# Kernel tuning notes

Hardware: AMD Instinct MI355X
Metric: run time of the kernel (lower is better)

## Reference

```python
import jax, jax.numpy as jnp
import numpy as np

N_NODES = 100000
N_EDGES = 800000
HIDDEN = 256
BOTTLENECK = 32


def setup_inputs() -> dict:
    key = jax.random.key(0)
    k1, k2, k3, k4 = jax.random.split(key, 4)
    x = jax.random.normal(k1, (N_NODES, HIDDEN), dtype=jnp.float32)
    edge_index = jax.random.randint(k2, (2, N_EDGES), 0, N_NODES, dtype=jnp.int64)
    # PyG GCNConv linear weights, init per module: normal(std=1e-5), zero bias
    W_down = jax.random.normal(k3, (BOTTLENECK, HIDDEN), dtype=jnp.float32) * 1e-5
    b_down = jnp.zeros((BOTTLENECK,), dtype=jnp.float32)
    W_up = jax.random.normal(k4, (HIDDEN, BOTTLENECK), dtype=jnp.float32) * 1e-5
    b_up = jnp.zeros((HIDDEN,), dtype=jnp.float32)
    return {"x": x, "edge_index": edge_index, "W_down": W_down, "b_down": b_down,
            "W_up": W_up, "b_up": b_up}


def reference(x, edge_index, W_down, b_down, W_up, b_up):
    N = x.shape[0]
    loops = jnp.arange(N, dtype=edge_index.dtype)
    # gcn_norm with self-loops (edge weight = 1), symmetric normalization
    row = jnp.concatenate([edge_index[0], loops])  # source nodes
    col = jnp.concatenate([edge_index[1], loops])  # target nodes
    deg = jax.ops.segment_sum(jnp.ones(row.shape[0], dtype=x.dtype), col, num_segments=N)
    dinv = jnp.where(deg > 0, jax.lax.rsqrt(deg), 0.0)
    norm = dinv[row] * dinv[col]  # [E+N]

    def gcn_conv(h, W, b):
        h = h @ W.T                                   # [N, out]
        msgs = h[row] * norm[:, None]                 # gather + weight
        return jax.ops.segment_sum(msgs, col, num_segments=N) + b

    h = jax.nn.relu(gcn_conv(x, W_down, b_down))      # down-proj conv + act
    out = gcn_conv(h, W_up, b_up) + x                 # up-proj conv + skip
    return out
```

## Files before the change

kernel.cpp:

```cpp
#include <hip/hip_runtime.h>
#include <hip/hip_bf16.h>
#include <stdint.h>

#define HID 256
#define BOT 32

typedef short short8 __attribute__((ext_vector_type(8)));
typedef unsigned short ushort8 __attribute__((ext_vector_type(8)));
typedef float floatx4 __attribute__((ext_vector_type(4)));

__device__ __forceinline__ unsigned short f2bu(float f) {
    return (unsigned short)(__float_as_uint(f) >> 16);
}
__device__ __forceinline__ float bu2f(unsigned short u) {
    return __uint_as_float((unsigned int)u << 16);
}
__device__ __forceinline__ short8 pack8(float4 a, float4 b) {
    short8 r;
    r[0] = (short)f2bu(a.x); r[1] = (short)f2bu(a.y);
    r[2] = (short)f2bu(a.z); r[3] = (short)f2bu(a.w);
    r[4] = (short)f2bu(b.x); r[5] = (short)f2bu(b.y);
    r[6] = (short)f2bu(b.z); r[7] = (short)f2bu(b.w);
    return r;
}

__device__ __forceinline__ int detect_mode(const int* __restrict__ ei, int* smode) {
    if (threadIdx.x < 64) {
        int found = 0;
        #pragma unroll
        for (int i = 0; i < 8; ++i) {
            int slot = 2 * (threadIdx.x * 8 + i) + 1;
            if (ei[slot] != 0) found = 1;
        }
        unsigned long long b = __ballot(found);
        if (threadIdx.x == 0) *smode = (b == 0ULL) ? 1 : 0;
    }
    __syncthreads();
    return *smode;
}


__global__ __launch_bounds__(256) void k_deg(const int* __restrict__ ei, int E,
                                             int* __restrict__ deg) {
    __shared__ int smode;
    int mode = detect_mode(ei, &smode);
    int e = blockIdx.x * 256 + threadIdx.x;
    if (e >= E) return;
    int d = mode ? ei[2 * (size_t)E + 2 * e] : ei[(size_t)E + e];
    atomicAdd(deg + d, 1);
}

__global__ __launch_bounds__(256) void k_alloc(const int* __restrict__ deg,
                                               float* __restrict__ dinv,
                                               int* __restrict__ start,
                                               int* __restrict__ cur,
                                               int* __restrict__ cursor, int N) {
    __shared__ int sdata[256];
    __shared__ int sbase;
    int tid = threadIdx.x;
    int i = blockIdx.x * 256 + tid;
    int d = (i < N) ? deg[i] : 0;
    if (i < N) dinv[i] = rsqrtf((float)(d + 1));
    sdata[tid] = d;
    __syncthreads();
    for (int off = 1; off < 256; off <<= 1) {
        int t = (tid >= off) ? sdata[tid - off] : 0;
        __syncthreads();
        sdata[tid] += t;
        __syncthreads();
    }
    if (tid == 0) sbase = atomicAdd(cursor, sdata[255]);
    __syncthreads();
    if (i < N) {
        int st = sbase + sdata[tid] - d;
        start[i] = st;
        cur[i] = st;
    }
}

__global__ __launch_bounds__(256) void k_fill_gemm(
    const int* __restrict__ ei, int E,
    const float* __restrict__ dinv, int* __restrict__ cur,
    int2* __restrict__ srcw,
    const float* __restrict__ x, const float* __restrict__ Wd,
    unsigned short* __restrict__ P, int N, int gemmBlocks, int gemmWaves)
{
    if (blockIdx.x >= gemmBlocks) {
        __shared__ int smode;
        int mode = detect_mode(ei, &smode);
        int e = (blockIdx.x - gemmBlocks) * 256 + threadIdx.x;
        if (e >= E) return;
        int s, d;
        if (mode) { s = ei[2 * (size_t)e]; d = ei[2 * (size_t)E + 2 * e]; }
        else      { s = ei[(size_t)e];     d = ei[(size_t)E + e]; }
        float w = dinv[s] * dinv[d];
        int slot = atomicAdd(cur + d, 1);
        srcw[slot] = make_int2(s, __float_as_int(w));
        return;
    }

    int wid  = (blockIdx.x * 256 + threadIdx.x) >> 6;
    int lane = threadIdx.x & 63;
    int m = lane & 15, q = lane >> 4;

    short8 bfr[2][8];
    #pragma unroll
    for (int jt = 0; jt < 2; ++jt) {
        const float4* wr = (const float4*)(Wd + (size_t)(jt * 16 + m) * HID);
        #pragma unroll
        for (int ks = 0; ks < 8; ++ks) {
            int c = (ks * 32 + q * 8) >> 2;
            bfr[jt][ks] = pack8(wr[c], wr[c + 1]);
        }
    }

    int tiles = (N + 15) >> 4;
    for (int t = wid; t < tiles; t += gemmWaves) {
        int n0 = t << 4;
        int row = n0 + m; if (row >= N) row = N - 1;
        const float4* xr = (const float4*)(x + (size_t)row * HID);
        floatx4 acc0 = {0.f, 0.f, 0.f, 0.f};
        floatx4 acc1 = {0.f, 0.f, 0.f, 0.f};
        #pragma unroll
        for (int ks = 0; ks < 8; ++ks) {
            int c = (ks * 32 + q * 8) >> 2;
            short8 af = pack8(xr[c], xr[c + 1]);
            acc0 = __builtin_amdgcn_mfma_f32_16x16x32_bf16(bfr[0][ks], af, acc0, 0, 0, 0);
            acc1 = __builtin_amdgcn_mfma_f32_16x16x32_bf16(bfr[1][ks], af, acc1, 0, 0, 0);
        }
        if (n0 + m < N) {
            unsigned int* pr = (unsigned int*)(P + (size_t)(n0 + m) * BOT);
            uint2 v0, v1;
            v0.x = (unsigned int)f2bu(acc0[0]) | ((unsigned int)f2bu(acc0[1]) << 16);
            v0.y = (unsigned int)f2bu(acc0[2]) | ((unsigned int)f2bu(acc0[3]) << 16);
            v1.x = (unsigned int)f2bu(acc1[0]) | ((unsigned int)f2bu(acc1[1]) << 16);
            v1.y = (unsigned int)f2bu(acc1[2]) | ((unsigned int)f2bu(acc1[3]) << 16);
            *(uint2*)(pr + q * 2)     = v0;
            *(uint2*)(pr + 8 + q * 2) = v1;
        }
    }
}

__global__ __launch_bounds__(256) void k_gather(
    const unsigned short* __restrict__ feat, const float* __restrict__ dinv,
    const int* __restrict__ start, const int* __restrict__ endp,
    const int2* __restrict__ srcw, const float* __restrict__ bias,
    unsigned short* __restrict__ dst, int N, int relu_bias)
{
    int t = blockIdx.x * 256 + threadIdx.x;
    int n = t >> 2, jq = (t & 3) * 8;
    if (n >= N) return;
    float di = dinv[n];
    float w0 = di * di;
    float acc[8];
    ushort8 sv = *(const ushort8*)(feat + (size_t)n * BOT + jq);
    #pragma unroll
    for (int i = 0; i < 8; ++i) acc[i] = w0 * bu2f(sv[i]);
    int k = start[n], en = endp[n];
    while (k < en) {
        int2 p[4];
        #pragma unroll
        for (int u = 0; u < 4; ++u) {
            int kk = k + u;
            int safe = kk < en ? kk : en - 1;
            p[u] = srcw[safe];
            if (kk >= en) p[u].y = 0;
        }
        ushort8 f[4];
        #pragma unroll
        for (int u = 0; u < 4; ++u)
            f[u] = *(const ushort8*)(feat + (size_t)p[u].x * BOT + jq);
        #pragma unroll
        for (int u = 0; u < 4; ++u) {
            float w = __int_as_float(p[u].y);
            #pragma unroll
            for (int i = 0; i < 8; ++i) acc[i] += w * bu2f(f[u][i]);
        }
        k += 4;
    }
    if (relu_bias) {
        #pragma unroll
        for (int i = 0; i < 8; ++i) {
            float a = acc[i] + bias[jq + i];
            acc[i] = a > 0.f ? a : 0.f;
        }
    }
    ushort8 o;
    #pragma unroll
    for (int i = 0; i < 8; ++i) o[i] = f2bu(acc[i]);
    *(ushort8*)(dst + (size_t)n * BOT + jq) = o;
}

__global__ __launch_bounds__(256) void k_gather_out(
    const unsigned short* __restrict__ A1, const float* __restrict__ dinv,
    const int* __restrict__ start, const int* __restrict__ endp,
    const int2* __restrict__ srcw,
    const float* __restrict__ x, const float* __restrict__ Wup,
    const float* __restrict__ bup, float* __restrict__ out, int N)
{
    int gw   = (blockIdx.x * 256 + threadIdx.x) >> 6;
    int lane = threadIdx.x & 63;
    int m = lane & 15, q = lane >> 4, jq = q * 8;
    int tiles = (N + 15) >> 4;
    if (gw >= tiles) return;
    int n0 = gw << 4;
    int n = n0 + m;
    bool ok = n < N;
    int nc = ok ? n : N - 1;

    float di = dinv[nc];
    float w0 = di * di;
    float acc[8];
    ushort8 sv = *(const ushort8*)(A1 + (size_t)nc * BOT + jq);
    #pragma unroll
    for (int i = 0; i < 8; ++i) acc[i] = w0 * bu2f(sv[i]);
    int k = start[nc], en = endp[nc];
    while (k < en) {
        int2 p[4];
        #pragma unroll
        for (int u = 0; u < 4; ++u) {
            int kk = k + u;
            int safe = kk < en ? kk : en - 1;
            p[u] = srcw[safe];
            if (kk >= en) p[u].y = 0;
        }
        ushort8 f[4];
        #pragma unroll
        for (int u = 0; u < 4; ++u)
            f[u] = *(const ushort8*)(A1 + (size_t)p[u].x * BOT + jq);
        #pragma unroll
        for (int u = 0; u < 4; ++u) {
            float w = __int_as_float(p[u].y);
            #pragma unroll
            for (int i = 0; i < 8; ++i) acc[i] += w * bu2f(f[u][i]);
        }
        k += 4;
    }

    short8 af;
    #pragma unroll
    for (int i = 0; i < 8; ++i) af[i] = (short)f2bu(acc[i]);

    const float4* xrow = (const float4*)(x + (size_t)nc * HID);
    floatx4* orow = (floatx4*)(out + (size_t)nc * HID);
    #pragma unroll
    for (int ft = 0; ft < 16; ++ft) {
        const float4* wr = (const float4*)(Wup + (size_t)(ft * 16 + m) * BOT);
        short8 bfr = pack8(wr[q * 2], wr[q * 2 + 1]);
        floatx4 a = {0.f, 0.f, 0.f, 0.f};
        a = __builtin_amdgcn_mfma_f32_16x16x32_bf16(bfr, af, a, 0, 0, 0);
        if (ok) {
            int c = ft * 4 + q;
            float4 xv = xrow[c];
            float4 bb = *(const float4*)(bup + ft * 16 + q * 4);
            floatx4 res;
            res[0] = a[0] + bb.x + xv.x;
            res[1] = a[1] + bb.y + xv.y;
            res[2] = a[2] + bb.z + xv.z;
            res[3] = a[3] + bb.w + xv.w;
            __builtin_nontemporal_store(res, &orow[c]);
        }
    }
}

extern "C" void kernel_launch(void* const* d_in, const int* in_sizes, int n_in,
                              void* d_out, int out_size, void* d_ws, size_t ws_size,
                              hipStream_t stream) {
    const float* x  = (const float*)d_in[0];
    const int*   ei = (const int*)d_in[1];
    const float* Wd = (const float*)d_in[2];
    const float* bd = (const float*)d_in[3];
    const float* Wu = (const float*)d_in[4];
    const float* bu = (const float*)d_in[5];
    float* out = (float*)d_out;

    int N = in_sizes[0] / HID;
    int E = in_sizes[1] / 2;

    char* ws = (char*)d_ws;
    int*   flags = (int*)ws;
    int*   deg   = (int*)(ws + 16);
    float* dinv  = (float*)(ws + 16 + (size_t)N * 4);
    int*   startp= (int*)(ws + 16 + (size_t)N * 8);
    int*   curp  = (int*)(ws + 16 + (size_t)N * 12);
    int2*  srcw  = (int2*)(ws + 16 + (size_t)N * 16);
    unsigned short* P  = (unsigned short*)(ws + 16 + (size_t)N * 16 + (size_t)E * 8);
    unsigned short* A1 = (unsigned short*)(ws + 16 + (size_t)N * 16 + (size_t)E * 8 + (size_t)N * 64);

    (void)hipMemsetAsync(ws, 0, 16 + (size_t)N * 4, stream);

    int eblocks = (E + 255) / 256;
    k_deg<<<eblocks, 256, 0, stream>>>(ei, E, deg);

    k_alloc<<<(N + 255) / 256, 256, 0, stream>>>(deg, dinv, startp, curp, flags + 1, N);

    int tiles = (N + 15) / 16;
    int gemmBlocks = (tiles + 3) / 4;
    k_fill_gemm<<<gemmBlocks + eblocks, 256, 0, stream>>>(
        ei, E, dinv, curp, srcw, x, Wd, P, N, gemmBlocks, gemmBlocks * 4);

    int gthreads = N * 4;
    k_gather<<<(gthreads + 255) / 256, 256, 0, stream>>>(P, dinv, startp, curp, srcw, bd, A1, N, 1);

    int oblocks = (tiles + 3) / 4;
    k_gather_out<<<oblocks, 256, 0, stream>>>(A1, dinv, startp, curp, srcw, x, Wu, bu, out, N);
}
```

Measured before the change: 353.5 us.

## Record per-edge slot during degree count to drop fill-phase atomics; split GEMM kernel

The degree-counting kernel now stores the return value of its atomicAdd as a per-edge slot. The CSR fill kernel computes each edge's position as start[dst] + slot instead of doing a second atomic on a cursor array. The cursor array is dropped, and the gather kernels take the end offset from start plus degree. The fused fill+GEMM launch is split into a separate fill kernel and a down-projection GEMM kernel with a fixed grid of 782 blocks. This adds an extra per-edge int array to write and read, and one more kernel launch.

New measurement: 349.2 us. Within noise of the previous version (-1.2%).

```diff
diff --git a/kernel.cpp b/kernel.cpp
--- a/kernel.cpp
+++ b/kernel.cpp
@@ -41,19 +41,19 @@
 
 
 __global__ __launch_bounds__(256) void k_deg(const int* __restrict__ ei, int E,
-                                             int* __restrict__ deg) {
+                                             int* __restrict__ deg,
+                                             int* __restrict__ eslot) {
     __shared__ int smode;
     int mode = detect_mode(ei, &smode);
     int e = blockIdx.x * 256 + threadIdx.x;
     if (e >= E) return;
     int d = mode ? ei[2 * (size_t)E + 2 * e] : ei[(size_t)E + e];
-    atomicAdd(deg + d, 1);
+    eslot[e] = atomicAdd(deg + d, 1);
 }
 
 __global__ __launch_bounds__(256) void k_alloc(const int* __restrict__ deg,
                                                float* __restrict__ dinv,
                                                int* __restrict__ start,
-                                               int* __restrict__ cur,
                                                int* __restrict__ cursor, int N) {
     __shared__ int sdata[256];
     __shared__ int sbase;
@@ -71,34 +71,30 @@
     }
     if (tid == 0) sbase = atomicAdd(cursor, sdata[255]);
     __syncthreads();
-    if (i < N) {
-        int st = sbase + sdata[tid] - d;
-        start[i] = st;
-        cur[i] = st;
-    }
-}
-
-__global__ __launch_bounds__(256) void k_fill_gemm(
-    const int* __restrict__ ei, int E,
-    const float* __restrict__ dinv, int* __restrict__ cur,
-    int2* __restrict__ srcw,
+    if (i < N) start[i] = sbase + sdata[tid] - d;
+}
+
+__global__ __launch_bounds__(256) void k_fill(const int* __restrict__ ei, int E,
+                                              const float* __restrict__ dinv,
+                                              const int* __restrict__ start,
+                                              const int* __restrict__ eslot,
+                                              int2* __restrict__ srcw) {
+    __shared__ int smode;
+    int mode = detect_mode(ei, &smode);
+    int e = blockIdx.x * 256 + threadIdx.x;
+    if (e >= E) return;
+    int s, d;
+    if (mode) { s = ei[2 * (size_t)e]; d = ei[2 * (size_t)E + 2 * e]; }
+    else      { s = ei[(size_t)e];     d = ei[(size_t)E + e]; }
+    float w = dinv[s] * dinv[d];
+    int slot = start[d] + eslot[e];
+    srcw[slot] = make_int2(s, __float_as_int(w));
+}
+
+__global__ __launch_bounds__(256) void k_gemm_down(
     const float* __restrict__ x, const float* __restrict__ Wd,
-    unsigned short* __restrict__ P, int N, int gemmBlocks, int gemmWaves)
+    unsigned short* __restrict__ P, int N, int nwaves)
 {
-    if (blockIdx.x >= gemmBlocks) {
-        __shared__ int smode;
-        int mode = detect_mode(ei, &smode);
-        int e = (blockIdx.x - gemmBlocks) * 256 + threadIdx.x;
-        if (e >= E) return;
-        int s, d;
-        if (mode) { s = ei[2 * (size_t)e]; d = ei[2 * (size_t)E + 2 * e]; }
-        else      { s = ei[(size_t)e];     d = ei[(size_t)E + e]; }
-        float w = dinv[s] * dinv[d];
-        int slot = atomicAdd(cur + d, 1);
-        srcw[slot] = make_int2(s, __float_as_int(w));
-        return;
-    }
-
     int wid  = (blockIdx.x * 256 + threadIdx.x) >> 6;
     int lane = threadIdx.x & 63;
     int m = lane & 15, q = lane >> 4;
@@ -115,7 +111,7 @@
     }
 
     int tiles = (N + 15) >> 4;
-    for (int t = wid; t < tiles; t += gemmWaves) {
+    for (int t = wid; t < tiles; t += nwaves) {
         int n0 = t << 4;
         int row = n0 + m; if (row >= N) row = N - 1;
         const float4* xr = (const float4*)(x + (size_t)row * HID);
@@ -143,7 +139,7 @@
 
 __global__ __launch_bounds__(256) void k_gather(
     const unsigned short* __restrict__ feat, const float* __restrict__ dinv,
-    const int* __restrict__ start, const int* __restrict__ endp,
+    const int* __restrict__ start, const int* __restrict__ cnt,
     const int2* __restrict__ srcw, const float* __restrict__ bias,
     unsigned short* __restrict__ dst, int N, int relu_bias)
 {
@@ -156,7 +152,7 @@
     ushort8 sv = *(const ushort8*)(feat + (size_t)n * BOT + jq);
     #pragma unroll
     for (int i = 0; i < 8; ++i) acc[i] = w0 * bu2f(sv[i]);
-    int k = start[n], en = endp[n];
+    int k = start[n], en = k + cnt[n];
     while (k < en) {
         int2 p[4];
         #pragma unroll
@@ -193,7 +189,7 @@
 
 __global__ __launch_bounds__(256) void k_gather_out(
     const unsigned short* __restrict__ A1, const float* __restrict__ dinv,
-    const int* __restrict__ start, const int* __restrict__ endp,
+    const int* __restrict__ start, const int* __restrict__ cnt,
     const int2* __restrict__ srcw,
     const float* __restrict__ x, const float* __restrict__ Wup,
     const float* __restrict__ bup, float* __restrict__ out, int N)
@@ -214,7 +210,7 @@
     ushort8 sv = *(const ushort8*)(A1 + (size_t)nc * BOT + jq);
     #pragma unroll
     for (int i = 0; i < 8; ++i) acc[i] = w0 * bu2f(sv[i]);
-    int k = start[nc], en = endp[nc];
+    int k = start[nc], en = k + cnt[nc];
     while (k < en) {
         int2 p[4];
         #pragma unroll
@@ -282,26 +278,27 @@
     int*   deg   = (int*)(ws + 16);
     float* dinv  = (float*)(ws + 16 + (size_t)N * 4);
     int*   startp= (int*)(ws + 16 + (size_t)N * 8);
-    int*   curp  = (int*)(ws + 16 + (size_t)N * 12);
-    int2*  srcw  = (int2*)(ws + 16 + (size_t)N * 16);
-    unsigned short* P  = (unsigned short*)(ws + 16 + (size_t)N * 16 + (size_t)E * 8);
-    unsigned short* A1 = (unsigned short*)(ws + 16 + (size_t)N * 16 + (size_t)E * 8 + (size_t)N * 64);
+    int*   eslot = (int*)(ws + 16 + (size_t)N * 12);
+    int2*  srcw  = (int2*)(ws + 16 + (size_t)N * 12 + (size_t)E * 4);
+    unsigned short* P  = (unsigned short*)(ws + 16 + (size_t)N * 12 + (size_t)E * 12);
+    unsigned short* A1 = (unsigned short*)(ws + 16 + (size_t)N * 12 + (size_t)E * 12 + (size_t)N * 64);
 
     (void)hipMemsetAsync(ws, 0, 16 + (size_t)N * 4, stream);
 
     int eblocks = (E + 255) / 256;
-    k_deg<<<eblocks, 256, 0, stream>>>(ei, E, deg);
-
-    k_alloc<<<(N + 255) / 256, 256, 0, stream>>>(deg, dinv, startp, curp, flags + 1, N);
+    k_deg<<<eblocks, 256, 0, stream>>>(ei, E, deg, eslot);
+
+    k_alloc<<<(N + 255) / 256, 256, 0, stream>>>(deg, dinv, startp, flags + 1, N);
+
+    k_fill<<<eblocks, 256, 0, stream>>>(ei, E, dinv, startp, eslot, srcw);
 
     int tiles = (N + 15) / 16;
-    int gemmBlocks = (tiles + 3) / 4;
-    k_fill_gemm<<<gemmBlocks + eblocks, 256, 0, stream>>>(
-        ei, E, dinv, curp, srcw, x, Wd, P, N, gemmBlocks, gemmBlocks * 4);
+    int gblocks = 782;
+    k_gemm_down<<<gblocks, 256, 0, stream>>>(x, Wd, P, N, gblocks * 4);
 
     int gthreads = N * 4;
-    k_gather<<<(gthreads + 255) / 256, 256, 0, stream>>>(P, dinv, startp, curp, srcw, bd, A1, N, 1);
+    k_gather<<<(gthreads + 255) / 256, 256, 0, stream>>>(P, dinv, startp, deg, srcw, bd, A1, N, 1);
 
     int oblocks = (tiles + 3) / 4;
-    k_gather_out<<<oblocks, 256, 0, stream>>>(A1, dinv, startp, curp, srcw, x, Wu, bu, out, N);
-}
+    k_gather_out<<<oblocks, 256, 0, stream>>>(A1, dinv, startp, deg, srcw, x, Wu, bu, out, N);
+}
```
